# Kernel optimization log

Hardware: AMD Instinct MI355X
Metric: run time of the kernel (lower is better)

The kernel has to match this reference:

```python
import jax, jax.numpy as jnp
import numpy as np

N_NODES = 50000
N_EDGES = 800000
EPS = 1e-5
NEG_SLOPE = 0.2


def _gatv2(x, src, dst, Wl, bl, Wr, br, att, bias, concat, N):
    # PyG GATv2Conv: xl = lin_l(x) (source side), xr = lin_r(x) (target side)
    H, C = att.shape
    xl = (x @ Wl + bl).reshape(N, H, C)
    xr = (x @ Wr + br).reshape(N, H, C)
    # per-edge message: leaky_relu(xl[j] + xr[i]), attention logit = <att, .>
    z = xl[src] + xr[dst]                      # [E, H, C]
    z = jnp.where(z > 0, z, NEG_SLOPE * z)
    logits = jnp.einsum('ehc,hc->eh', z, att)  # [E, H]
    # segment softmax over incoming edges of each target node
    m = jax.lax.stop_gradient(jax.ops.segment_max(logits, dst, num_segments=N))
    p = jnp.exp(logits - m[dst])
    s = jax.ops.segment_sum(p, dst, num_segments=N)
    alpha = p / s[dst]                         # [E, H]
    out = jax.ops.segment_sum(xl[src] * alpha[..., None], dst, num_segments=N)  # [N, H, C]
    out = out.reshape(N, H * C) if concat else out.mean(axis=1)
    return out + bias


def _bn(x, g, b):
    mu = x.mean(axis=0)
    v = x.var(axis=0)
    return (x - mu) * jax.lax.rsqrt(v + EPS) * g + b


def setup_inputs() -> dict:
    key = jax.random.key(0)
    ks = jax.random.split(key, 16)
    x = jax.random.normal(ks[0], (N_NODES, 2), jnp.float32)
    edge_index = jax.random.randint(ks[1], (2, N_EDGES), 0, N_NODES, dtype=jnp.int64)

    def lin(k, i, o):
        return jax.random.normal(k, (i, o), jnp.float32) * (1.0 / np.sqrt(i))

    inp = {'x': x, 'edge_index': edge_index}
    # layer 1: in=2, heads=8, out=16, concat
    inp['W1l'] = lin(ks[2], 2, 128); inp['b1l'] = jnp.zeros((128,), jnp.float32)
    inp['W1r'] = lin(ks[3], 2, 128); inp['b1r'] = jnp.zeros((128,), jnp.float32)
    inp['a1'] = jax.random.normal(ks[4], (8, 16), jnp.float32) * 0.1
    inp['bias1'] = jnp.zeros((128,), jnp.float32)
    inp['g1'] = jnp.ones((128,), jnp.float32); inp['be1'] = jnp.zeros((128,), jnp.float32)
    # layer 2: in=128, heads=4, out=16, concat
    inp['W2l'] = lin(ks[5], 128, 64); inp['b2l'] = jnp.zeros((64,), jnp.float32)
    inp['W2r'] = lin(ks[6], 128, 64); inp['b2r'] = jnp.zeros((64,), jnp.float32)
    inp['a2'] = jax.random.normal(ks[7], (4, 16), jnp.float32) * 0.1
    inp['bias2'] = jnp.zeros((64,), jnp.float32)
    inp['g2'] = jnp.ones((64,), jnp.float32); inp['be2'] = jnp.zeros((64,), jnp.float32)
    # layer 3: in=64, heads=1, out=2, mean (concat=False)
    inp['W3l'] = lin(ks[8], 64, 2); inp['b3l'] = jnp.zeros((2,), jnp.float32)
    inp['W3r'] = lin(ks[9], 64, 2); inp['b3r'] = jnp.zeros((2,), jnp.float32)
    inp['a3'] = jax.random.normal(ks[10], (1, 2), jnp.float32) * 0.1
    inp['bias3'] = jnp.zeros((2,), jnp.float32)
    return inp


def reference(x, edge_index, W1l, b1l, W1r, b1r, a1, bias1, g1, be1,
              W2l, b2l, W2r, b2r, a2, bias2, g2, be2,
              W3l, b3l, W3r, b3r, a3, bias3):
    N = x.shape[0]
    loops = jnp.arange(N, dtype=edge_index.dtype)
    src = jnp.concatenate([edge_index[0], loops])  # add self loops (PyG default)
    dst = jnp.concatenate([edge_index[1], loops])
    h = _gatv2(x, src, dst, W1l, b1l, W1r, b1r, a1, bias1, True, N)
    h = jax.nn.elu(_bn(h, g1, be1))  # dropout is identity in eval
    h = _gatv2(h, src, dst, W2l, b2l, W2r, b2r, a2, bias2, True, N)
    h = jax.nn.elu(_bn(h, g2, be2))
    return _gatv2(h, src, dst, W3l, b3l, W3r, b3r, a3, bias3, False, N)
```

## Files before the change

kernel.cpp:

```cpp
#include <hip/hip_runtime.h>
#include <hip/hip_bf16.h>

#define N_NODES 50000
#define N_E0    800000
#define N_ET    850000
#define EPSBN   1e-5f
#define LOG2E   1.4426950408889634f

#define LEAKY(z) fmaxf((z), 0.2f * (z))

#define OFF_C 0
#define OFF_A (128*N_NODES)
#define OFF_B (192*N_NODES)
#define OFF_STATS (256*N_NODES)
#define OFF_S1R (OFF_STATS + 512)
#define OFF_S2R (OFF_S1R + 16384)
#define OFF_P (OFF_S2R + 8192)
#define N_PARAM_TOT 118312
#define OFF_ROWPTR (OFF_P + N_PARAM_TOT)
#define OFF_DEG    (OFF_ROWPTR + 50001)
#define OFF_CURSOR (OFF_DEG + 50000)
#define OFF_BSUM   (OFF_CURSOR + 50000)
#define OFF_COL    (OFF_BSUM + 256)
#define OFF_FLAGS  (OFF_COL + 850064)
#define OFF_SCNT   (OFF_FLAGS + 2)

#define BK_CAP 131072
#define BK_CHUNK 2048

__device__ __forceinline__ float bf2f(unsigned short u) {
    return __uint_as_float(((unsigned int)u) << 16);
}
__device__ __forceinline__ unsigned short f2bf(float f) {
    unsigned int u = __float_as_uint(f);
    u += 0x7FFFu + ((u >> 16) & 1u);
    return (unsigned short)(u >> 16);
}

__global__ void prep_kernel(const unsigned short* xr, const int* ei, int* flags,
                            int* deg, float* stats, float* s1r, float* s2r, int* scnt) {
    int i = blockIdx.x * 256 + threadIdx.x;
    if (i < N_NODES) deg[i] = 0;
    if (i < 512) stats[i] = 0.f;
    if (i < 16384) s1r[i] = 0.f;
    if (i < 8192)  s2r[i] = 0.f;
    if (i < 8) scnt[i] = 0;
    if (blockIdx.x == 0) {
        __shared__ int c1, c2;
        if (threadIdx.x == 0) { c1 = 0; c2 = 0; }
        __syncthreads();
        int t = threadIdx.x;
        int l1 = 0, l2 = 0;
        for (int k = t; k < 2048; k += 256) {
            float v = bf2f(xr[k]);
            if (!(fabsf(v) <= 100.0f)) l1++;
            if (ei[2 * k + 1] != 0) l2++;
        }
        atomicAdd(&c1, l1);
        atomicAdd(&c2, l2);
        __syncthreads();
        if (t == 0) {
            flags[0] = (c1 > 16) ? 1 : 0;
            flags[1] = (c2 == 0) ? 1 : 0;
        }
    }
}

struct ParamPtrs { const void* p[23]; };

__global__ void convert_kernel(ParamPtrs ps, float* dst, const int* flags) {
    const int sizes[23] = {100000, 256,128,256,128,128,128,128,128,
                           8192,64,8192,64,64,64,64,64,
                           128,2,128,2,2,2};
    int g = blockIdx.x * 256 + threadIdx.x;
    if (g >= N_PARAM_TOT) return;
    int t = 0, off = g;
    while (off >= sizes[t]) { off -= sizes[t]; t++; }
    float v;
    if (flags[0]) v = ((const float*)ps.p[t])[off];
    else          v = bf2f(((const unsigned short*)ps.p[t])[off]);
    if (t == 5 || t == 13 || t == 21) v *= LOG2E;
    dst[g] = v;
}

__global__ void bucket_kernel(const int* ei, const int* flags, int* scnt,
                              int* dstb, int* srcb, int* deg) {
    __shared__ int lcnt[8];
    __shared__ int lbase[8];
    int tid = threadIdx.x;
    if (tid < 8) lcnt[tid] = 0;
    __syncthreads();
    int base_e = blockIdx.x * BK_CHUNK;
    int i64 = flags[1];
    int src[8], dst[8], pos[8];
    #pragma unroll
    for (int u = 0; u < 8; u++) {
        int e = base_e + u * 256 + tid;
        if (e < N_ET) {
            int s, d;
            if (e < N_E0) {
                d = i64 ? ei[2 * (N_E0 + e)] : ei[N_E0 + e];
                s = i64 ? ei[2 * e] : ei[e];
            } else { s = d = e - N_E0; }
            src[u] = s; dst[u] = d;
            pos[u] = atomicAdd(&lcnt[d / 6250], 1);
            atomicAdd(&deg[d], 1);
        } else dst[u] = -1;
    }
    __syncthreads();
    if (tid < 8) lbase[tid] = atomicAdd(&scnt[tid], lcnt[tid]);
    __syncthreads();
    #pragma unroll
    for (int u = 0; u < 8; u++) {
        if (dst[u] >= 0) {
            int st = dst[u] / 6250;
            int gp = st * BK_CAP + lbase[st] + pos[u];
            dstb[gp] = dst[u];
            srcb[gp] = src[u];
        }
    }
}

__global__ void scan1_kernel(const int* deg, int* row_ptr, int* bsum) {
    __shared__ int sh[256];
    int i = blockIdx.x * 256 + threadIdx.x;
    int v = (i < N_NODES) ? deg[i] : 0;
    sh[threadIdx.x] = v;
    __syncthreads();
    for (int off = 1; off < 256; off <<= 1) {
        int t = (threadIdx.x >= off) ? sh[threadIdx.x - off] : 0;
        __syncthreads();
        sh[threadIdx.x] += t;
        __syncthreads();
    }
    if (i < N_NODES) row_ptr[i] = sh[threadIdx.x] - v;
    if (threadIdx.x == 255) bsum[blockIdx.x] = sh[255];
}

__global__ void scan23_kernel(int* row_ptr, int* cursor, const int* bsum) {
    __shared__ int sh[256];
    int t = threadIdx.x;
    int v = (t < 196) ? bsum[t] : 0;
    sh[t] = v;
    __syncthreads();
    for (int off = 1; off < 256; off <<= 1) {
        int u = (t >= off) ? sh[t - off] : 0;
        __syncthreads();
        sh[t] += u;
        __syncthreads();
    }
    int prefix = (blockIdx.x == 0) ? 0 : sh[blockIdx.x - 1];
    int i = blockIdx.x * 256 + t;
    if (i < N_NODES) {
        int r = row_ptr[i] + prefix;
        row_ptr[i] = r;
        cursor[i] = r;
    }
    if (i == 0) row_ptr[N_NODES] = N_ET;
}

__global__ void scatter2_kernel(const int* scnt, const int* dstb, const int* srcb,
                                int* cursor, int* col) {
    int stripe = blockIdx.x & 7;
    int bi = blockIdx.x >> 3;
    int cnt = scnt[stripe];
    int off = stripe * BK_CAP;
    for (int t = bi * 256 + threadIdx.x; t < cnt; t += 32 * 256) {
        int d = dstb[off + t];
        int pos = atomicAdd(&cursor[d], 1);
        col[pos] = srcb[off + t];
    }
}

__global__ void __launch_bounds__(256) gather1_kernel(
    const int* row_ptr, const int* col, const float* x,
    const float* W1l, const float* b1l, const float* W1r, const float* b1r,
    const float* att, const float* bias, unsigned int* Cb, float* s1r)
{
    int gid = blockIdx.x * 256 + threadIdx.x;
    int n = gid >> 6;
    int lane = threadIdx.x & 63;
    float2 wl0 = *(const float2*)(W1l + 2 * lane);
    float2 wl1 = *(const float2*)(W1l + 128 + 2 * lane);
    float2 bl  = *(const float2*)(b1l + 2 * lane);
    float2 wr0 = *(const float2*)(W1r + 2 * lane);
    float2 wr1 = *(const float2*)(W1r + 128 + 2 * lane);
    float2 br  = *(const float2*)(b1r + 2 * lane);
    float2 at  = *(const float2*)(att + 2 * lane);
    float2 xd  = *(const float2*)(x + 2 * n);
    float xr0 = fmaf(xd.x, wr0.x, fmaf(xd.y, wr1.x, br.x));
    float xr1 = fmaf(xd.x, wr0.y, fmaf(xd.y, wr1.y, br.y));
    int base = __builtin_amdgcn_readfirstlane(row_ptr[n]);
    int deg  = __builtin_amdgcn_readfirstlane(row_ptr[n + 1]) - base;
    float acc0 = 0.f, acc1 = 0.f, den = 0.f;
    for (int j0 = 0; j0 < deg; j0 += 64) {
        int cnt = deg - j0; if (cnt > 64) cnt = 64;
        int msrc = col[base + j0 + lane];
        int j = 0;
        for (; j + 8 <= cnt; j += 8) {
            int s[8];
            #pragma unroll
            for (int u = 0; u < 8; u++) s[u] = __builtin_amdgcn_readlane(msrc, j + u);
            float2 xs[8];
            #pragma unroll
            for (int u = 0; u < 8; u++) xs[u] = *(const float2*)(x + 2 * s[u]);
            float xl0[8], xl1[8], part[8];
            #pragma unroll
            for (int u = 0; u < 8; u++) {
                xl0[u] = fmaf(xs[u].x, wl0.x, fmaf(xs[u].y, wl1.x, bl.x));
                xl1[u] = fmaf(xs[u].x, wl0.y, fmaf(xs[u].y, wl1.y, bl.y));
                float z0 = LEAKY(xl0[u] + xr0);
                float z1 = LEAKY(xl1[u] + xr1);
                part[u] = fmaf(z0, at.x, z1 * at.y);
            }
            #pragma unroll
            for (int m = 1; m <= 4; m <<= 1) {
                #pragma unroll
                for (int u = 0; u < 8; u++) part[u] += __shfl_xor(part[u], m, 64);
            }
            #pragma unroll
            for (int u = 0; u < 8; u++) {
                float p = exp2f(part[u]);
                acc0 = fmaf(p, xl0[u], acc0);
                acc1 = fmaf(p, xl1[u], acc1);
                den += p;
            }
        }
        for (; j < cnt; ++j) {
            int s0 = __builtin_amdgcn_readlane(msrc, j);
            float2 xs = *(const float2*)(x + 2 * s0);
            float xl0s = fmaf(xs.x, wl0.x, fmaf(xs.y, wl1.x, bl.x));
            float xl1s = fmaf(xs.x, wl0.y, fmaf(xs.y, wl1.y, bl.y));
            float z0 = LEAKY(xl0s + xr0);
            float z1 = LEAKY(xl1s + xr1);
            float part = fmaf(z0, at.x, z1 * at.y);
            part += __shfl_xor(part, 1, 64);
            part += __shfl_xor(part, 2, 64);
            part += __shfl_xor(part, 4, 64);
            float p = exp2f(part);
            acc0 = fmaf(p, xl0s, acc0);
            acc1 = fmaf(p, xl1s, acc1);
            den += p;
        }
    }
    float inv = 1.f / den;
    float2 bi = *(const float2*)(bias + 2 * lane);
    float2 outv;
    outv.x = fmaf(acc0, inv, bi.x);
    outv.y = fmaf(acc1, inv, bi.y);
    Cb[n * 64 + lane] = ((unsigned int)f2bf(outv.y) << 16) | f2bf(outv.x);
    __shared__ float sred[4][128];
    __shared__ float qred[4][128];
    int wv = threadIdx.x >> 6;
    sred[wv][2 * lane]     = outv.x;
    sred[wv][2 * lane + 1] = outv.y;
    qred[wv][2 * lane]     = outv.x * outv.x;
    qred[wv][2 * lane + 1] = outv.y * outv.y;
    __syncthreads();
    int t = threadIdx.x;
    float a;
    if (t < 128) a = sred[0][t] + sred[1][t] + sred[2][t] + sred[3][t];
    else { int c = t - 128; a = qred[0][c] + qred[1][c] + qred[2][c] + qred[3][c]; }
    atomicAdd(&s1r[(blockIdx.x & 63) * 256 + t], a);
}

__global__ void red1_kernel(const float* s1r, const float* g1, const float* be1,
                            float* stats) {
    __shared__ float ls[256];
    int t = threadIdx.x;
    float a = 0.f;
    for (int r = 0; r < 64; r++) a += s1r[r * 256 + t];
    ls[t] = a;
    __syncthreads();
    if (t < 128) {
        float mu = ls[t] * (1.0f / N_NODES);
        float var = ls[128 + t] * (1.0f / N_NODES) - mu * mu;
        float sc = g1[t] * rsqrtf(var + EPSBN);
        stats[t] = sc;
        stats[128 + t] = be1[t] - mu * sc;
    }
}

__global__ void __launch_bounds__(256) lin2_kernel(
    const unsigned int* Cb, const float* stats, const float* Wl, const float* bl,
    const float* Wr, const float* br, unsigned short* xl2b, float* xr2)
{
    __shared__ float h[64 * 132];
    int tid = threadIdx.x;
    int nb = blockIdx.x * 64;
    for (int i = tid; i < 64 * 64; i += 256) {
        int ni = i >> 6, kp = i & 63;
        int n = nb + ni;
        int k = 2 * kp;
        float v0 = 0.f, v1 = 0.f;
        if (n < N_NODES) {
            unsigned int pk = Cb[n * 64 + kp];
            float b0 = fmaf(__uint_as_float(pk << 16),        stats[k],     stats[128 + k]);
            float b1 = fmaf(__uint_as_float(pk & 0xffff0000u), stats[k + 1], stats[128 + k + 1]);
            v0 = b0 > 0.f ? b0 : __expf(b0) - 1.f;
            v1 = b1 > 0.f ? b1 : __expf(b1) - 1.f;
        }
        h[ni * 132 + k]     = v0;
        h[ni * 132 + k + 1] = v1;
    }
    __syncthreads();
    int kt = (tid & 15) * 4;
    int nt = (tid >> 4) * 4;
    float accl[4][4], accr[4][4];
    #pragma unroll
    for (int i = 0; i < 4; i++) {
        #pragma unroll
        for (int k = 0; k < 4; k++) { accl[i][k] = 0.f; accr[i][k] = 0.f; }
    }
    for (int j = 0; j < 128; j += 4) {
        float4 hv[4];
        #pragma unroll
        for (int i = 0; i < 4; i++)
            hv[i] = *(const float4*)&h[(nt + i) * 132 + j];
        #pragma unroll
        for (int jj = 0; jj < 4; jj++) {
            float4 wl4 = *(const float4*)&Wl[(j + jj) * 64 + kt];
            float4 wr4 = *(const float4*)&Wr[(j + jj) * 64 + kt];
            #pragma unroll
            for (int i = 0; i < 4; i++) {
                float hvv = (jj == 0) ? hv[i].x : (jj == 1) ? hv[i].y :
                            (jj == 2) ? hv[i].z : hv[i].w;
                accl[i][0] += hvv * wl4.x; accl[i][1] += hvv * wl4.y;
                accl[i][2] += hvv * wl4.z; accl[i][3] += hvv * wl4.w;
                accr[i][0] += hvv * wr4.x; accr[i][1] += hvv * wr4.y;
                accr[i][2] += hvv * wr4.z; accr[i][3] += hvv * wr4.w;
            }
        }
    }
    float4 blv = *(const float4*)&bl[kt];
    float4 brv = *(const float4*)&br[kt];
    #pragma unroll
    for (int i = 0; i < 4; i++) {
        int n = nb + nt + i;
        if (n < N_NODES) {
            ushort4 ob;
            ob.x = f2bf(accl[i][0] + blv.x);
            ob.y = f2bf(accl[i][1] + blv.y);
            ob.z = f2bf(accl[i][2] + blv.z);
            ob.w = f2bf(accl[i][3] + blv.w);
            *(ushort4*)&xl2b[n * 64 + kt] = ob;
            float4 o;
            o.x = accr[i][0] + brv.x; o.y = accr[i][1] + brv.y;
            o.z = accr[i][2] + brv.z; o.w = accr[i][3] + brv.w;
            *(float4*)&xr2[n * 64 + kt] = o;
        }
    }
}

__global__ void __launch_bounds__(256) gather2_kernel(
    const int* row_ptr, const int* col, const unsigned short* xl2b, const float* xr2,
    const float* att, const float* bias, float* C, float* s2r)
{
    int gid = blockIdx.x * 256 + threadIdx.x;
    int n = gid >> 6;
    int lane = threadIdx.x & 63;
    int grp = lane >> 4;
    int cidx = lane & 15;
    float4 xrv = *(const float4*)(xr2 + n * 64 + 4 * cidx);
    float4 atv = *(const float4*)(att + 4 * cidx);
    int base = __builtin_amdgcn_readfirstlane(row_ptr[n]);
    int deg  = __builtin_amdgcn_readfirstlane(row_ptr[n + 1]) - base;
    float4 acc = make_float4(0.f, 0.f, 0.f, 0.f);
    float den = 0.f;
    for (int j0 = 0; j0 < deg; j0 += 64) {
        int cnt = deg - j0; if (cnt > 64) cnt = 64;
        int msrc = col[base + j0 + lane];
        for (int j4 = 0; j4 < cnt; j4 += 8) {
            int e0 = j4 + grp, e1 = j4 + 4 + grp;
            int s0 = __shfl(msrc, e0, 64);
            int s1 = __shfl(msrc, e1, 64);
            bool v0 = e0 < cnt, v1 = e1 < cnt;
            s0 = v0 ? s0 : 0;
            s1 = v1 ? s1 : 0;
            uint2 ba = *(const uint2*)(xl2b + (size_t)s0 * 64 + 4 * cidx);
            uint2 bb = *(const uint2*)(xl2b + (size_t)s1 * 64 + 4 * cidx);
            float a0 = __uint_as_float(ba.x << 16);
            float a1 = __uint_as_float(ba.x & 0xffff0000u);
            float a2 = __uint_as_float(ba.y << 16);
            float a3 = __uint_as_float(ba.y & 0xffff0000u);
            float b0 = __uint_as_float(bb.x << 16);
            float b1 = __uint_as_float(bb.x & 0xffff0000u);
            float b2 = __uint_as_float(bb.y << 16);
            float b3 = __uint_as_float(bb.y & 0xffff0000u);
            float pa = LEAKY(a0 + xrv.x) * atv.x;
            pa = fmaf(LEAKY(a1 + xrv.y), atv.y, pa);
            pa = fmaf(LEAKY(a2 + xrv.z), atv.z, pa);
            pa = fmaf(LEAKY(a3 + xrv.w), atv.w, pa);
            float pb = LEAKY(b0 + xrv.x) * atv.x;
            pb = fmaf(LEAKY(b1 + xrv.y), atv.y, pb);
            pb = fmaf(LEAKY(b2 + xrv.z), atv.z, pb);
            pb = fmaf(LEAKY(b3 + xrv.w), atv.w, pb);
            pa += __shfl_xor(pa, 1, 64);
            pa += __shfl_xor(pa, 2, 64);
            pb += __shfl_xor(pb, 1, 64);
            pb += __shfl_xor(pb, 2, 64);
            float ea = v0 ? exp2f(pa) : 0.f;
            float eb = v1 ? exp2f(pb) : 0.f;
            acc.x = fmaf(ea, a0, acc.x); acc.x = fmaf(eb, b0, acc.x);
            acc.y = fmaf(ea, a1, acc.y); acc.y = fmaf(eb, b1, acc.y);
            acc.z = fmaf(ea, a2, acc.z); acc.z = fmaf(eb, b2, acc.z);
            acc.w = fmaf(ea, a3, acc.w); acc.w = fmaf(eb, b3, acc.w);
            den += ea + eb;
        }
    }
    acc.x += __shfl_xor(acc.x, 16, 64); acc.x += __shfl_xor(acc.x, 32, 64);
    acc.y += __shfl_xor(acc.y, 16, 64); acc.y += __shfl_xor(acc.y, 32, 64);
    acc.z += __shfl_xor(acc.z, 16, 64); acc.z += __shfl_xor(acc.z, 32, 64);
    acc.w += __shfl_xor(acc.w, 16, 64); acc.w += __shfl_xor(acc.w, 32, 64);
    den += __shfl_xor(den, 16, 64);
    den += __shfl_xor(den, 32, 64);
    float inv = 1.f / den;
    float4 bi = *(const float4*)(bias + 4 * cidx);
    float4 o;
    o.x = fmaf(acc.x, inv, bi.x);
    o.y = fmaf(acc.y, inv, bi.y);
    o.z = fmaf(acc.z, inv, bi.z);
    o.w = fmaf(acc.w, inv, bi.w);
    if (lane < 16) *(float4*)(C + n * 64 + 4 * cidx) = o;
    __shared__ float sred[4][64];
    __shared__ float qred[4][64];
    int wv = threadIdx.x >> 6;
    if (lane < 16) {
        int c = 4 * cidx;
        sred[wv][c]     = o.x; qred[wv][c]     = o.x * o.x;
        sred[wv][c + 1] = o.y; qred[wv][c + 1] = o.y * o.y;
        sred[wv][c + 2] = o.z; qred[wv][c + 2] = o.z * o.z;
        sred[wv][c + 3] = o.w; qred[wv][c + 3] = o.w * o.w;
    }
    __syncthreads();
    int t = threadIdx.x;
    if (t < 128) {
        float a;
        if (t < 64) a = sred[0][t] + sred[1][t] + sred[2][t] + sred[3][t];
        else { int c = t - 64; a = qred[0][c] + qred[1][c] + qred[2][c] + qred[3][c]; }
        atomicAdd(&s2r[(blockIdx.x & 63) * 128 + t], a);
    }
}

__global__ void red2_kernel(const float* s2r, const float* g2, const float* be2,
                            float* stats) {
    __shared__ float ls[128];
    int t = threadIdx.x;
    float a = 0.f;
    for (int r = 0; r < 64; r++) a += s2r[r * 128 + t];
    ls[t] = a;
    __syncthreads();
    if (t < 64) {
        float mu = ls[t] * (1.0f / N_NODES);
        float var = ls[64 + t] * (1.0f / N_NODES) - mu * mu;
        float sc = g2[t] * rsqrtf(var + EPSBN);
        stats[t] = sc;
        stats[64 + t] = be2[t] - mu * sc;
    }
}

__global__ void __launch_bounds__(256) lin3_kernel(
    const float* C, const float* stats2,
    const float* Wl, const float* bl, const float* Wr, const float* br,
    float* xl3, float* xr3)
{
    int gid = blockIdx.x * 256 + threadIdx.x;
    int n = gid >> 6;
    int lane = threadIdx.x & 63;
    if (n >= N_NODES) return;
    float v = fmaf(C[n * 64 + lane], stats2[lane], stats2[64 + lane]);
    float h = v > 0.f ? v : __expf(v) - 1.f;
    float2 wlv = *(const float2*)(Wl + 2 * lane);
    float2 wrv = *(const float2*)(Wr + 2 * lane);
    float a0 = h * wlv.x, a1 = h * wlv.y;
    float r0 = h * wrv.x, r1 = h * wrv.y;
    #pragma unroll
    for (int m = 1; m < 64; m <<= 1) {
        a0 += __shfl_xor(a0, m, 64);
        a1 += __shfl_xor(a1, m, 64);
        r0 += __shfl_xor(r0, m, 64);
        r1 += __shfl_xor(r1, m, 64);
    }
    if (lane == 0) {
        xl3[2 * n]     = a0 + bl[0];
        xl3[2 * n + 1] = a1 + bl[1];
        xr3[2 * n]     = r0 + br[0];
        xr3[2 * n + 1] = r1 + br[1];
    }
}

__global__ void __launch_bounds__(256) gather3_kernel(
    const int* row_ptr, const int* col,
    const float* xl3, const float* xr3,
    const float* att, const float* bias,
    void* out, const int* flags) {
    int gid = blockIdx.x * 256 + threadIdx.x;
    int n = gid >> 2;
    int q = threadIdx.x & 3;
    if (n >= N_NODES) return;
    float a0 = att[0], a1 = att[1];
    float xr0 = xr3[2 * n], xr1 = xr3[2 * n + 1];
    float acc0 = 0.f, acc1 = 0.f, den = 0.f;
    int e0 = row_ptr[n], e1 = row_ptr[n + 1];
    for (int e = e0 + q; e < e1; e += 4) {
        int src = col[e];
        float2 xs = *(const float2*)(xl3 + 2 * src);
        float z0 = LEAKY(xs.x + xr0);
        float z1 = LEAKY(xs.y + xr1);
        float p = exp2f(fmaf(z0, a0, z1 * a1));
        acc0 = fmaf(p, xs.x, acc0);
        acc1 = fmaf(p, xs.y, acc1);
        den += p;
    }
    acc0 += __shfl_xor(acc0, 1, 64); acc0 += __shfl_xor(acc0, 2, 64);
    acc1 += __shfl_xor(acc1, 1, 64); acc1 += __shfl_xor(acc1, 2, 64);
    den  += __shfl_xor(den, 1, 64);  den  += __shfl_xor(den, 2, 64);
    if (q == 0) {
        float inv = 1.f / den;
        float v0 = fmaf(acc0, inv, bias[0]);
        float v1 = fmaf(acc1, inv, bias[1]);
        if (flags[0]) {
            ((float*)out)[2 * n] = v0;
            ((float*)out)[2 * n + 1] = v1;
        } else {
            ((__hip_bfloat16*)out)[2 * n] = __float2bfloat16(v0);
            ((__hip_bfloat16*)out)[2 * n + 1] = __float2bfloat16(v1);
        }
    }
}

extern "C" void kernel_launch(void* const* d_in, const int* in_sizes, int n_in,
                              void* d_out, int out_size, void* d_ws, size_t ws_size,
                              hipStream_t stream) {
    float* W = (float*)d_ws;
    float* C = W + OFF_C;
    float* A = W + OFF_A;
    float* B = W + OFF_B;
    float* STATS = W + OFF_STATS;
    float* S1R = W + OFF_S1R;
    float* S2R = W + OFF_S2R;
    float* P = W + OFF_P;
    int* ROWPTR = (int*)(W + OFF_ROWPTR);
    int* DEG    = (int*)(W + OFF_DEG);
    int* CURSOR = (int*)(W + OFF_CURSOR);
    int* BSUM   = (int*)(W + OFF_BSUM);
    int* COL    = (int*)(W + OFF_COL);
    int* FLAGS  = (int*)(W + OFF_FLAGS);
    int* SCNT   = (int*)(W + OFF_SCNT);
    int* DSTB   = (int*)(W + OFF_C);
    int* SRCB   = DSTB + 8 * BK_CAP;

    const int* ei = (const int*)d_in[1];

    float* Px  = P;
    float* W1l = Px + 100000; float* b1l = W1l + 256; float* W1r = b1l + 128; float* b1r = W1r + 256;
    float* a1  = b1r + 128;   float* bias1 = a1 + 128; float* g1 = bias1 + 128; float* be1 = g1 + 128;
    float* W2l = be1 + 128;   float* b2l = W2l + 8192; float* W2r = b2l + 64;  float* b2r = W2r + 8192;
    float* a2  = b2r + 64;    float* bias2 = a2 + 64;  float* g2 = bias2 + 64; float* be2 = g2 + 64;
    float* W3l = be2 + 64;    float* b3l = W3l + 128;  float* W3r = b3l + 2;   float* b3r = W3r + 128;
    float* a3  = b3r + 2;     float* bias3 = a3 + 2;

    prep_kernel<<<196, 256, 0, stream>>>((const unsigned short*)d_in[0], ei, FLAGS, DEG, STATS, S1R, S2R, SCNT);

    ParamPtrs ps;
    ps.p[0] = d_in[0];
    for (int j = 1; j < 23; j++) ps.p[j] = d_in[j + 1];
    convert_kernel<<<(N_PARAM_TOT + 255) / 256, 256, 0, stream>>>(ps, P, FLAGS);

    bucket_kernel<<<(N_ET + BK_CHUNK - 1) / BK_CHUNK, 256, 0, stream>>>(ei, FLAGS, SCNT, DSTB, SRCB, DEG);
    scan1_kernel<<<196, 256, 0, stream>>>(DEG, ROWPTR, BSUM);
    scan23_kernel<<<196, 256, 0, stream>>>(ROWPTR, CURSOR, BSUM);
    scatter2_kernel<<<256, 256, 0, stream>>>(SCNT, DSTB, SRCB, CURSOR, COL);

    gather1_kernel<<<N_NODES * 64 / 256, 256, 0, stream>>>(ROWPTR, COL, Px, W1l, b1l, W1r, b1r, a1, bias1, (unsigned int*)C, S1R);
    red1_kernel<<<1, 256, 0, stream>>>(S1R, g1, be1, STATS);

    lin2_kernel<<<(N_NODES + 63) / 64, 256, 0, stream>>>((const unsigned int*)C, STATS, W2l, b2l, W2r, b2r, (unsigned short*)A, B);
    gather2_kernel<<<N_NODES * 64 / 256, 256, 0, stream>>>(ROWPTR, COL, (const unsigned short*)A, B, a2, bias2, C, S2R);
    red2_kernel<<<1, 128, 0, stream>>>(S2R, g2, be2, STATS + 256);

    lin3_kernel<<<N_NODES * 64 / 256, 256, 0, stream>>>(C, STATS + 256, W3l, b3l, W3r, b3r, A, B);
    gather3_kernel<<<(N_NODES * 4 + 255) / 256, 256, 0, stream>>>(ROWPTR, COL, A, B, a3, bias3, d_out, FLAGS);
}
```

Baseline: 333.1 us.

## Restructure layer-1 gather: aggregate raw 2-D inputs, apply lin_l after softmax

The layer-1 gather now exploits linearity: instead of aggregating the 128-wide projected source features, it aggregates only the two raw input coordinates weighted by the softmax and applies W1l afterwards. Each wave processes 8 edges in parallel (8 lanes per edge, one lane per head with 16 channels), so cross-lane shuffles per edge disappear, and the partial sums are reduced across edge groups at the end. This cuts per-edge ALU work and shuffles. In exchange each lane holds more weights in registers, and padding zeros are written after the column array so the overrun reads stay in bounds.

```diff
diff --git a/kernel.cpp b/kernel.cpp
--- a/kernel.cpp
+++ b/kernel.cpp
@@ -28,6 +28,16 @@
 #define BK_CAP 131072
 #define BK_CHUNK 2048
 
+typedef float v2f __attribute__((ext_vector_type(2)));
+
+__device__ __forceinline__ v2f ld2(const float* p) { return *(const v2f*)p; }
+__device__ __forceinline__ v2f fma2(v2f a, v2f b, v2f c) {
+    return __builtin_elementwise_fma(a, b, c);
+}
+__device__ __forceinline__ v2f max2(v2f a, v2f b) {
+    return __builtin_elementwise_max(a, b);
+}
+
 __device__ __forceinline__ float bf2f(unsigned short u) {
     return __uint_as_float(((unsigned int)u) << 16);
 }
@@ -38,13 +48,15 @@
 }
 
 __global__ void prep_kernel(const unsigned short* xr, const int* ei, int* flags,
-                            int* deg, float* stats, float* s1r, float* s2r, int* scnt) {
+                            int* deg, float* stats, float* s1r, float* s2r, int* scnt,
+                            int* col) {
     int i = blockIdx.x * 256 + threadIdx.x;
     if (i < N_NODES) deg[i] = 0;
     if (i < 512) stats[i] = 0.f;
     if (i < 16384) s1r[i] = 0.f;
     if (i < 8192)  s2r[i] = 0.f;
     if (i < 8) scnt[i] = 0;
+    if (i < 64) col[N_ET + i] = 0;
     if (blockIdx.x == 0) {
         __shared__ int c1, c2;
         if (threadIdx.x == 0) { c1 = 0; c2 = 0; }
@@ -180,82 +192,75 @@
     int gid = blockIdx.x * 256 + threadIdx.x;
     int n = gid >> 6;
     int lane = threadIdx.x & 63;
-    float2 wl0 = *(const float2*)(W1l + 2 * lane);
-    float2 wl1 = *(const float2*)(W1l + 128 + 2 * lane);
-    float2 bl  = *(const float2*)(b1l + 2 * lane);
-    float2 wr0 = *(const float2*)(W1r + 2 * lane);
-    float2 wr1 = *(const float2*)(W1r + 128 + 2 * lane);
-    float2 br  = *(const float2*)(b1r + 2 * lane);
-    float2 at  = *(const float2*)(att + 2 * lane);
-    float2 xd  = *(const float2*)(x + 2 * n);
-    float xr0 = fmaf(xd.x, wr0.x, fmaf(xd.y, wr1.x, br.x));
-    float xr1 = fmaf(xd.x, wr0.y, fmaf(xd.y, wr1.y, br.y));
+    int g = lane >> 3;
+    int h = lane & 7;
+    int c0 = h << 4;
+
+    v2f w0[8], w1[8], at[8], K[8];
+    v2f xd = ld2(x + 2 * n);
+    v2f xdx = {xd.x, xd.x}, xdy = {xd.y, xd.y};
+    #pragma unroll
+    for (int k = 0; k < 8; k++) {
+        w0[k] = ld2(W1l + c0 + 2 * k);
+        w1[k] = ld2(W1l + 128 + c0 + 2 * k);
+        at[k] = ld2(att + c0 + 2 * k);
+        v2f wr0 = ld2(W1r + c0 + 2 * k);
+        v2f wr1 = ld2(W1r + 128 + c0 + 2 * k);
+        v2f bb  = ld2(b1r + c0 + 2 * k) + ld2(b1l + c0 + 2 * k);
+        K[k] = fma2(xdx, wr0, fma2(xdy, wr1, bb));
+    }
+
     int base = __builtin_amdgcn_readfirstlane(row_ptr[n]);
     int deg  = __builtin_amdgcn_readfirstlane(row_ptr[n + 1]) - base;
-    float acc0 = 0.f, acc1 = 0.f, den = 0.f;
-    for (int j0 = 0; j0 < deg; j0 += 64) {
-        int cnt = deg - j0; if (cnt > 64) cnt = 64;
-        int msrc = col[base + j0 + lane];
-        int j = 0;
-        for (; j + 8 <= cnt; j += 8) {
-            int s[8];
-            #pragma unroll
-            for (int u = 0; u < 8; u++) s[u] = __builtin_amdgcn_readlane(msrc, j + u);
-            float2 xs[8];
-            #pragma unroll
-            for (int u = 0; u < 8; u++) xs[u] = *(const float2*)(x + 2 * s[u]);
-            float xl0[8], xl1[8], part[8];
-            #pragma unroll
-            for (int u = 0; u < 8; u++) {
-                xl0[u] = fmaf(xs[u].x, wl0.x, fmaf(xs[u].y, wl1.x, bl.x));
-                xl1[u] = fmaf(xs[u].x, wl0.y, fmaf(xs[u].y, wl1.y, bl.y));
-                float z0 = LEAKY(xl0[u] + xr0);
-                float z1 = LEAKY(xl1[u] + xr1);
-                part[u] = fmaf(z0, at.x, z1 * at.y);
-            }
-            #pragma unroll
-            for (int m = 1; m <= 4; m <<= 1) {
-                #pragma unroll
-                for (int u = 0; u < 8; u++) part[u] += __shfl_xor(part[u], m, 64);
-            }
-            #pragma unroll
-            for (int u = 0; u < 8; u++) {
-                float p = exp2f(part[u]);
-                acc0 = fmaf(p, xl0[u], acc0);
-                acc1 = fmaf(p, xl1[u], acc1);
-                den += p;
-            }
-        }
-        for (; j < cnt; ++j) {
-            int s0 = __builtin_amdgcn_readlane(msrc, j);
-            float2 xs = *(const float2*)(x + 2 * s0);
-            float xl0s = fmaf(xs.x, wl0.x, fmaf(xs.y, wl1.x, bl.x));
-            float xl1s = fmaf(xs.x, wl0.y, fmaf(xs.y, wl1.y, bl.y));
-            float z0 = LEAKY(xl0s + xr0);
-            float z1 = LEAKY(xl1s + xr1);
-            float part = fmaf(z0, at.x, z1 * at.y);
-            part += __shfl_xor(part, 1, 64);
-            part += __shfl_xor(part, 2, 64);
-            part += __shfl_xor(part, 4, 64);
-            float p = exp2f(part);
-            acc0 = fmaf(p, xl0s, acc0);
-            acc1 = fmaf(p, xl1s, acc1);
-            den += p;
-        }
-    }
-    float inv = 1.f / den;
-    float2 bi = *(const float2*)(bias + 2 * lane);
-    float2 outv;
-    outv.x = fmaf(acc0, inv, bi.x);
-    outv.y = fmaf(acc1, inv, bi.y);
-    Cb[n * 64 + lane] = ((unsigned int)f2bf(outv.y) << 16) | f2bf(outv.x);
+
+    float S0 = 0.f, S1 = 0.f, SP = 0.f;
+    for (int j0 = 0; j0 < deg; j0 += 8) {
+        int e = j0 + g;
+        int s = col[base + e];
+        v2f xs = ld2(x + 2 * s);
+        v2f x0 = {xs.x, xs.x}, x1 = {xs.y, xs.y};
+        v2f lgA = {0.f, 0.f}, lgB = {0.f, 0.f};
+        #pragma unroll
+        for (int k = 0; k < 8; k += 2) {
+            v2f t = fma2(x1, w1[k],     fma2(x0, w0[k],     K[k]));
+            lgA = fma2(max2(t, 0.2f * t), at[k], lgA);
+            v2f u = fma2(x1, w1[k + 1], fma2(x0, w0[k + 1], K[k + 1]));
+            lgB = fma2(max2(u, 0.2f * u), at[k + 1], lgB);
+        }
+        v2f lg = lgA + lgB;
+        float logit = lg.x + lg.y;
+        float p = (e < deg) ? exp2f(logit) : 0.f;
+        S0 = fmaf(p, xs.x, S0);
+        S1 = fmaf(p, xs.y, S1);
+        SP += p;
+    }
+
+    #pragma unroll
+    for (int m = 8; m <= 32; m <<= 1) {
+        S0 += __shfl_xor(S0, m, 64);
+        S1 += __shfl_xor(S1, m, 64);
+        SP += __shfl_xor(SP, m, 64);
+    }
+    float inv = 1.f / SP;
+    float t0 = S0 * inv, t1 = S1 * inv;
+
+    int hsrc = lane >> 3;
+    float t0o = __shfl(t0, hsrc, 64);
+    float t1o = __shfl(t1, hsrc, 64);
+    v2f w0o = ld2(W1l + 2 * lane);
+    v2f w1o = ld2(W1l + 128 + 2 * lane);
+    v2f bo  = ld2(b1l + 2 * lane) + ld2(bias + 2 * lane);
+    float ox = fmaf(w0o.x, t0o, fmaf(w1o.x, t1o, bo.x));
+    float oy = fmaf(w0o.y, t0o, fmaf(w1o.y, t1o, bo.y));
+    Cb[n * 64 + lane] = ((unsigned int)f2bf(oy) << 16) | f2bf(ox);
+
     __shared__ float sred[4][128];
     __shared__ float qred[4][128];
     int wv = threadIdx.x >> 6;
-    sred[wv][2 * lane]     = outv.x;
-    sred[wv][2 * lane + 1] = outv.y;
-    qred[wv][2 * lane]     = outv.x * outv.x;
-    qred[wv][2 * lane + 1] = outv.y * outv.y;
+    sred[wv][2 * lane]     = ox;
+    sred[wv][2 * lane + 1] = oy;
+    qred[wv][2 * lane]     = ox * ox;
+    qred[wv][2 * lane + 1] = oy * oy;
     __syncthreads();
     int t = threadIdx.x;
     float a;
@@ -560,7 +565,7 @@
     float* W3l = be2 + 64;    float* b3l = W3l + 128;  float* W3r = b3l + 2;   float* b3r = W3r + 128;
     float* a3  = b3r + 2;     float* bias3 = a3 + 2;
 
-    prep_kernel<<<196, 256, 0, stream>>>((const unsigned short*)d_in[0], ei, FLAGS, DEG, STATS, S1R, S2R, SCNT);
+    prep_kernel<<<196, 256, 0, stream>>>((const unsigned short*)d_in[0], ei, FLAGS, DEG, STATS, S1R, S2R, SCNT, COL);
 
     ParamPtrs ps;
     ps.p[0] = d_in[0];
```

Measured after the change: 402.1 us. 1.21x slower.
